# Kernel optimization log

Hardware: AMD Instinct MI355X
Metric: run time of the kernel (lower is better)

The kernel has to match this reference:

```python
import jax, jax.numpy as jnp
import numpy as np

N, E, D = 50000, 800000, 128
EPS = 1e-5


def _layernorm(x, g, b):
    m = jnp.mean(x, axis=-1, keepdims=True)
    v = jnp.mean((x - m) ** 2, axis=-1, keepdims=True)
    return (x - m) * jax.lax.rsqrt(v + EPS) * g + b


def setup_inputs() -> dict:
    key = jax.random.key(0)
    ks = jax.random.split(key, 8)
    x = jax.random.normal(ks[0], (N, D), dtype=jnp.float32)
    edge_index = jax.random.randint(ks[1], (2, E), 0, N, dtype=jnp.int64)
    edge_weights = jax.random.uniform(ks[2], (E,), dtype=jnp.float32)
    s = 1.0 / np.sqrt(D)
    W1 = jax.random.uniform(ks[3], (D, D), minval=-s, maxval=s, dtype=jnp.float32)
    b1 = jax.random.uniform(ks[4], (D,), minval=-s, maxval=s, dtype=jnp.float32)
    W2 = jax.random.uniform(ks[5], (D, D), minval=-s, maxval=s, dtype=jnp.float32)
    b2 = jax.random.uniform(ks[6], (D,), minval=-s, maxval=s, dtype=jnp.float32)
    g1 = jnp.ones((D,), jnp.float32); be1 = jnp.zeros((D,), jnp.float32)
    g2 = jnp.ones((D,), jnp.float32); be2 = jnp.zeros((D,), jnp.float32)
    return {"x": x, "edge_index": edge_index, "edge_weights": edge_weights,
            "W1": W1, "b1": b1, "g1": g1, "be1": be1,
            "W2": W2, "b2": b2, "g2": g2, "be2": be2}


def _layer(x, src, dst, ew, W, b, g, be):
    h = jax.nn.relu(x @ W + b)                      # [N, D]
    msg = ew[:, None] * h[src]                      # [E, D] gather
    h = h + jax.ops.segment_sum(msg, dst, num_segments=N)  # scatter-add (matches serial loop)
    return _layernorm(h, g, be)                     # dropout is identity at inference


def reference(x, edge_index, edge_weights, W1, b1, g1, be1, W2, b2, g2, be2):
    src, dst = edge_index[0], edge_index[1]
    x = _layer(x, src, dst, edge_weights, W1, b1, g1, be1)
    x = _layer(x, src, dst, edge_weights, W2, b2, g2, be2)
    return x
```

## Files before the change

kernel.cpp:

```cpp
#include <hip/hip_runtime.h>
#include <hip/hip_bf16.h>


#define D 128
#define SA 8192

typedef __attribute__((ext_vector_type(8))) short short8;
typedef __attribute__((ext_vector_type(4))) float f32x4;

__global__ __launch_bounds__(1024) void k_zero(int* __restrict__ p, int m) {
    int i = blockIdx.x * 1024 + threadIdx.x;
    if (i < m) p[i] = 0;
}

__global__ __launch_bounds__(1024) void k_bhist(const int* __restrict__ dst, int e,
                                                int n, int nb,
                                                int* __restrict__ bhist) {
    __shared__ int lh[784];
    int tid = threadIdx.x;
    for (int i = tid; i < nb; i += 1024) lh[i] = 0;
    __syncthreads();
    int i0 = blockIdx.x * SA;
#pragma unroll
    for (int k = 0; k < SA / 1024; ++k) {
        int i = i0 + k * 1024 + tid;
        if (i < e) {
            int d = dst[i];
            d = min(max(d, 0), n - 1);
            atomicAdd(&lh[d >> 6], 1);
        }
    }
    __syncthreads();
    for (int i = tid; i < nb; i += 1024)
        if (lh[i]) atomicAdd(&bhist[i], lh[i]);
}

__global__ __launch_bounds__(1024) void k_bscan(const int* __restrict__ bhist, int nb,
                                                int* __restrict__ boff,
                                                int* __restrict__ bcursor) {
    __shared__ int s[1024];
    int t = threadIdx.x;
    int v = (t < nb) ? bhist[t] : 0;
    s[t] = v;
    __syncthreads();
    for (int off = 1; off < 1024; off <<= 1) {
        int u = (t >= off) ? s[t - off] : 0;
        __syncthreads();
        s[t] += u;
        __syncthreads();
    }
    if (t < nb) {
        int ex = s[t] - v;
        boff[t] = ex;
        bcursor[t] = ex;
    }
}

__global__ __launch_bounds__(1024) void k_bfill(const int* __restrict__ src,
                                                const int* __restrict__ dst,
                                                const float* __restrict__ ew, int e,
                                                int n, int nb,
                                                int* __restrict__ bcursor,
                                                uint2* __restrict__ csr_tmp) {
    __shared__ int lh[784];
    __shared__ int gbase[784];
    int tid = threadIdx.x;
    for (int i = tid; i < nb; i += 1024) lh[i] = 0;
    __syncthreads();
    int i0 = blockIdx.x * SA;
    int bkt[SA / 1024], pos[SA / 1024];
    unsigned pk[SA / 1024];
    float wv[SA / 1024];
#pragma unroll
    for (int k = 0; k < SA / 1024; ++k) {
        int i = i0 + k * 1024 + tid;
        bkt[k] = -1;
        if (i < e) {
            int d = dst[i];
            d = min(max(d, 0), n - 1);
            int s = src[i];
            s = min(max(s, 0), n - 1);
            int b = d >> 6;
            bkt[k] = b;
            pos[k] = atomicAdd(&lh[b], 1);
            pk[k] = (unsigned)s | ((unsigned)(d & 63) << 16);
            wv[k] = ew[i];
        }
    }
    __syncthreads();
    for (int i = tid; i < nb; i += 1024)
        gbase[i] = lh[i] ? atomicAdd(&bcursor[i], lh[i]) : 0;
    __syncthreads();
#pragma unroll
    for (int k = 0; k < SA / 1024; ++k) {
        if (bkt[k] >= 0) {
            int idx = gbase[bkt[k]] + pos[k];
            csr_tmp[idx] = make_uint2(pk[k], __float_as_uint(wv[k]));
        }
    }
}

__global__ __launch_bounds__(256) void k_bfinal(const uint2* __restrict__ csr_tmp,
                                                const int* __restrict__ boff, int n,
                                                int e, int nb,
                                                int* __restrict__ row_ptr,
                                                uint2* __restrict__ csr) {
    __shared__ int dh[64], dcur[64], dscan[64];
    int b = blockIdx.x;
    int tid = threadIdx.x;
    int base = boff[b];
    int endo = (b + 1 < nb) ? boff[b + 1] : e;
    int ndst = min(64, n - b * 64);
    if (tid < 64) { dh[tid] = 0; dcur[tid] = 0; }
    __syncthreads();
    for (int i = base + tid; i < endo; i += 256) {
        unsigned u = csr_tmp[i].x;
        atomicAdd(&dh[(u >> 16) & 63], 1);
    }
    __syncthreads();
    if (tid < 64) {
        int v = dh[tid];
        int incl = v;
#pragma unroll
        for (int off = 1; off < 64; off <<= 1) {
            int u = __shfl_up(incl, off, 64);
            if (tid >= off) incl += u;
        }
        dscan[tid] = incl - v;
        if (tid < ndst) row_ptr[b * 64 + tid] = base + incl - v;
        if (b == nb - 1 && tid == 0) row_ptr[n] = e;
    }
    __syncthreads();
    for (int i = base + tid; i < endo; i += 256) {
        uint2 en = csr_tmp[i];
        int dlo = (en.x >> 16) & 63;
        int p = atomicAdd(&dcur[dlo], 1);
        csr[base + dscan[dlo] + p] = en;
    }
}

__global__ __launch_bounds__(256) void k_wprep(const float* __restrict__ W1,
                                               const float* __restrict__ W2,
                                               short* __restrict__ WT1,
                                               short* __restrict__ WT2) {
    int b = blockIdx.x;
    const float* W = (b < 64) ? W1 : W2;
    short* WT = (b < 64) ? WT1 : WT2;
    int i = (b & 63) * 256 + threadIdx.x;
    int k = i >> 7, nn = i & 127;
    WT[nn * 128 + k] = (short)__bfloat16_as_ushort(__float2bfloat16(W[i]));
}

__device__ __forceinline__ short8 cvt8(const float* p) {
    float4 v0 = *(const float4*)p;
    float4 v1 = *(const float4*)(p + 4);
    short8 r;
    r[0] = (short)__bfloat16_as_ushort(__float2bfloat16(v0.x));
    r[1] = (short)__bfloat16_as_ushort(__float2bfloat16(v0.y));
    r[2] = (short)__bfloat16_as_ushort(__float2bfloat16(v0.z));
    r[3] = (short)__bfloat16_as_ushort(__float2bfloat16(v0.w));
    r[4] = (short)__bfloat16_as_ushort(__float2bfloat16(v1.x));
    r[5] = (short)__bfloat16_as_ushort(__float2bfloat16(v1.y));
    r[6] = (short)__bfloat16_as_ushort(__float2bfloat16(v1.z));
    r[7] = (short)__bfloat16_as_ushort(__float2bfloat16(v1.w));
    return r;
}

template <int F32IN>
__global__ __launch_bounds__(256, 2) void k_gemm_mfma(const float* __restrict__ xf,
                                                      const short* __restrict__ xb,
                                                      const short* __restrict__ WT,
                                                      const float* __restrict__ bias,
                                                      ushort* __restrict__ hb, int n) {
    int lane = threadIdx.x & 63;
    int wid = threadIdx.x >> 6;
    int ln = lane & 15, g = lane >> 4;
    short8 bfr[8][4];
#pragma unroll
    for (int nt = 0; nt < 8; ++nt)
#pragma unroll
        for (int kk = 0; kk < 4; ++kk)
            bfr[nt][kk] = *(const short8*)(WT + (nt * 16 + ln) * 128 + kk * 32 + g * 8);
    float bvv[8];
#pragma unroll
    for (int nt = 0; nt < 8; ++nt) bvv[nt] = bias[nt * 16 + ln];

    int ntile = n >> 4;
    int stride = gridDim.x * 4;
    for (int t = blockIdx.x * 4 + wid; t < ntile; t += stride) {
        int row = t * 16 + ln;
        short8 a[4];
        if (F32IN) {
            const float* px = xf + (size_t)row * 128 + g * 8;
            a[0] = cvt8(px);
            a[1] = cvt8(px + 32);
            a[2] = cvt8(px + 64);
            a[3] = cvt8(px + 96);
        } else {
            const short* px = xb + (size_t)row * 128 + g * 8;
            a[0] = *(const short8*)(px);
            a[1] = *(const short8*)(px + 32);
            a[2] = *(const short8*)(px + 64);
            a[3] = *(const short8*)(px + 96);
        }
        f32x4 acc[8] = {};
#pragma unroll
        for (int kk = 0; kk < 4; ++kk)
#pragma unroll
            for (int nt = 0; nt < 8; ++nt)
                acc[nt] = __builtin_amdgcn_mfma_f32_16x16x32_bf16(a[kk], bfr[nt][kk],
                                                                  acc[nt], 0, 0, 0);
        int r0 = t * 16 + g * 4;
#pragma unroll
        for (int nt = 0; nt < 8; ++nt) {
#pragma unroll
            for (int r = 0; r < 4; ++r) {
                float v = fmaxf(acc[nt][r] + bvv[nt], 0.0f);
                hb[(size_t)(r0 + r) * 128 + nt * 16 + ln] =
                    __bfloat16_as_ushort(__float2bfloat16(v));
            }
        }
    }
}

__device__ __forceinline__ void bf2_unpack(unsigned int u, float& lo, float& hi) {
    lo = __uint_as_float(u << 16);
    hi = __uint_as_float(u & 0xffff0000u);
}

__global__ __launch_bounds__(256) void k_aggln(const unsigned int* __restrict__ hb,
                                               const float2* __restrict__ g2,
                                               const float2* __restrict__ be2,
                                               const int* __restrict__ row_ptr,
                                               const uint2* __restrict__ csr,
                                               float2* __restrict__ out2,
                                               unsigned int* __restrict__ xb_out,
                                               int n) {
    int wid = threadIdx.x >> 6;
    int lane = threadIdx.x & 63;
    int node = blockIdx.x * 4 + wid;
    if (node >= n) return;
    float ax, ay;
    bf2_unpack(hb[node * 64 + lane], ax, ay);
    int beg = row_ptr[node], end = row_ptr[node + 1];
    int j = beg;
    for (; j + 8 <= end; j += 8) {
        uint2 e0 = csr[j + 0], e1 = csr[j + 1], e2 = csr[j + 2], e3 = csr[j + 3];
        uint2 e4 = csr[j + 4], e5 = csr[j + 5], e6 = csr[j + 6], e7 = csr[j + 7];
        unsigned int u0 = hb[(e0.x & 0xffffu) * 64 + lane];
        unsigned int u1 = hb[(e1.x & 0xffffu) * 64 + lane];
        unsigned int u2 = hb[(e2.x & 0xffffu) * 64 + lane];
        unsigned int u3 = hb[(e3.x & 0xffffu) * 64 + lane];
        unsigned int u4 = hb[(e4.x & 0xffffu) * 64 + lane];
        unsigned int u5 = hb[(e5.x & 0xffffu) * 64 + lane];
        unsigned int u6 = hb[(e6.x & 0xffffu) * 64 + lane];
        unsigned int u7 = hb[(e7.x & 0xffffu) * 64 + lane];
        float lx, ly;
        bf2_unpack(u0, lx, ly); ax += __uint_as_float(e0.y) * lx; ay += __uint_as_float(e0.y) * ly;
        bf2_unpack(u1, lx, ly); ax += __uint_as_float(e1.y) * lx; ay += __uint_as_float(e1.y) * ly;
        bf2_unpack(u2, lx, ly); ax += __uint_as_float(e2.y) * lx; ay += __uint_as_float(e2.y) * ly;
        bf2_unpack(u3, lx, ly); ax += __uint_as_float(e3.y) * lx; ay += __uint_as_float(e3.y) * ly;
        bf2_unpack(u4, lx, ly); ax += __uint_as_float(e4.y) * lx; ay += __uint_as_float(e4.y) * ly;
        bf2_unpack(u5, lx, ly); ax += __uint_as_float(e5.y) * lx; ay += __uint_as_float(e5.y) * ly;
        bf2_unpack(u6, lx, ly); ax += __uint_as_float(e6.y) * lx; ay += __uint_as_float(e6.y) * ly;
        bf2_unpack(u7, lx, ly); ax += __uint_as_float(e7.y) * lx; ay += __uint_as_float(e7.y) * ly;
    }
    for (; j + 4 <= end; j += 4) {
        uint2 e0 = csr[j + 0], e1 = csr[j + 1], e2 = csr[j + 2], e3 = csr[j + 3];
        unsigned int u0 = hb[(e0.x & 0xffffu) * 64 + lane];
        unsigned int u1 = hb[(e1.x & 0xffffu) * 64 + lane];
        unsigned int u2 = hb[(e2.x & 0xffffu) * 64 + lane];
        unsigned int u3 = hb[(e3.x & 0xffffu) * 64 + lane];
        float lx, ly;
        bf2_unpack(u0, lx, ly); ax += __uint_as_float(e0.y) * lx; ay += __uint_as_float(e0.y) * ly;
        bf2_unpack(u1, lx, ly); ax += __uint_as_float(e1.y) * lx; ay += __uint_as_float(e1.y) * ly;
        bf2_unpack(u2, lx, ly); ax += __uint_as_float(e2.y) * lx; ay += __uint_as_float(e2.y) * ly;
        bf2_unpack(u3, lx, ly); ax += __uint_as_float(e3.y) * lx; ay += __uint_as_float(e3.y) * ly;
    }
    for (; j < end; ++j) {
        uint2 e0 = csr[j];
        float lx, ly;
        bf2_unpack(hb[(e0.x & 0xffffu) * 64 + lane], lx, ly);
        ax += __uint_as_float(e0.y) * lx;
        ay += __uint_as_float(e0.y) * ly;
    }
    float sum = ax + ay;
#pragma unroll
    for (int m = 1; m < 64; m <<= 1) sum += __shfl_xor(sum, m, 64);
    float mean = sum * (1.0f / 128.0f);
    float dx = ax - mean, dy = ay - mean;
    float ss = dx * dx + dy * dy;
#pragma unroll
    for (int m = 1; m < 64; m <<= 1) ss += __shfl_xor(ss, m, 64);
    float rstd = rsqrtf(ss * (1.0f / 128.0f) + 1e-5f);
    float2 gg = g2[lane], bb = be2[lane];
    float2 o;
    o.x = dx * rstd * gg.x + bb.x;
    o.y = dy * rstd * gg.y + bb.y;
    out2[node * 64 + lane] = o;
    if (xb_out) {
        unsigned int u = (unsigned int)__bfloat16_as_ushort(__float2bfloat16(o.x)) |
                         ((unsigned int)__bfloat16_as_ushort(__float2bfloat16(o.y)) << 16);
        xb_out[node * 64 + lane] = u;
    }
}

extern "C" void kernel_launch(void* const* d_in, const int* in_sizes, int n_in,
                              void* d_out, int out_size, void* d_ws, size_t ws_size,
                              hipStream_t stream) {
    const float* x   = (const float*)d_in[0];
    const int*  eidx = (const int*)d_in[1];
    const float* ew  = (const float*)d_in[2];
    const float* W1  = (const float*)d_in[3];
    const float* b1  = (const float*)d_in[4];
    const float* g1  = (const float*)d_in[5];
    const float* be1 = (const float*)d_in[6];
    const float* W2  = (const float*)d_in[7];
    const float* b2  = (const float*)d_in[8];
    const float* g2  = (const float*)d_in[9];
    const float* be2 = (const float*)d_in[10];
    int n = in_sizes[0] / D;
    int e = in_sizes[2];
    const int* srcp = eidx;
    const int* dstp = eidx + e;
    float* out = (float*)d_out;

    char* ws = (char*)d_ws;
    size_t off = 0;
    auto alloc = [&](size_t bytes) {
        void* p = ws + off;
        off += (bytes + 255) & ~(size_t)255;
        return p;
    };
    ushort* hb      = (ushort*)alloc((size_t)n * D * sizeof(ushort));
    uint*   xb      = (uint*)alloc((size_t)n * (D / 2) * sizeof(uint));
    int*    row_ptr = (int*)alloc((size_t)(n + 1) * sizeof(int));
    int*    bhist   = (int*)alloc(1024 * sizeof(int));
    int*    boff    = (int*)alloc(1024 * sizeof(int));
    int*    bcursor = (int*)alloc(1024 * sizeof(int));
    short*  WT1     = (short*)alloc(128 * 128 * sizeof(short));
    short*  WT2     = (short*)alloc(128 * 128 * sizeof(short));
    uint2*  csr_tmp = (uint2*)alloc((size_t)e * sizeof(uint2));
    uint2*  csr     = (uint2*)alloc((size_t)e * sizeof(uint2));

    int nb = (n + 63) >> 6;
    int nblk = (e + SA - 1) / SA;

    k_zero<<<1, 1024, 0, stream>>>(bhist, nb);
    k_wprep<<<128, 256, 0, stream>>>(W1, W2, WT1, WT2);
    k_bhist<<<nblk, 1024, 0, stream>>>(dstp, e, n, nb, bhist);
    k_bscan<<<1, 1024, 0, stream>>>(bhist, nb, boff, bcursor);
    k_bfill<<<nblk, 1024, 0, stream>>>(srcp, dstp, ew, e, n, nb, bcursor, csr_tmp);
    k_bfinal<<<nb, 256, 0, stream>>>(csr_tmp, boff, n, e, nb, row_ptr, csr);

    k_gemm_mfma<1><<<512, 256, 0, stream>>>(x, nullptr, WT1, b1, hb, n);
    k_aggln<<<(n + 3) / 4, 256, 0, stream>>>((const unsigned int*)hb,
                                             (const float2*)g1, (const float2*)be1,
                                             row_ptr, csr, (float2*)out, xb, n);
    k_gemm_mfma<0><<<512, 256, 0, stream>>>(nullptr, (const short*)xb, WT2, b2, hb, n);
    k_aggln<<<(n + 3) / 4, 256, 0, stream>>>((const unsigned int*)hb,
                                             (const float2*)g2, (const float2*)be2,
                                             row_ptr, csr, (float2*)out, nullptr, n);
}
```

Before: 146.1 us.

## Merge prep kernels, use nontemporal loads/stores, split GEMM N-tiles across waves

Fuses the histogram-zeroing and weight-transpose launches into one kernel. Switches streaming loads and stores in the CSR build, GEMM and aggregation to nontemporal builtins. Restructures the MFMA GEMM so the four waves of a block share one 16-row tile, each computing two 16-column output tiles, with the grid doubled. The first layer's aggregation also skips its redundant fp32 output write. Together these aim to cut launch overhead, cache pollution, register pressure and wasted writes, at the cost of more blocks and the A tile being reloaded by each wave.

```diff
diff --git a/kernel.cpp b/kernel.cpp
--- a/kernel.cpp
+++ b/kernel.cpp
@@ -7,10 +7,24 @@
 
 typedef __attribute__((ext_vector_type(8))) short short8;
 typedef __attribute__((ext_vector_type(4))) float f32x4;
-
-__global__ __launch_bounds__(1024) void k_zero(int* __restrict__ p, int m) {
-    int i = blockIdx.x * 1024 + threadIdx.x;
-    if (i < m) p[i] = 0;
+typedef __attribute__((ext_vector_type(2))) float f32x2;
+typedef __attribute__((ext_vector_type(2))) unsigned int uint2v;
+
+__global__ __launch_bounds__(256) void k_prep(const float* __restrict__ W1,
+                                              const float* __restrict__ W2,
+                                              short* __restrict__ WT1,
+                                              short* __restrict__ WT2,
+                                              int* __restrict__ bhist, int nb) {
+    int b = blockIdx.x;
+    if (b < 128) {
+        const float* W = (b < 64) ? W1 : W2;
+        short* WT = (b < 64) ? WT1 : WT2;
+        int i = (b & 63) * 256 + threadIdx.x;
+        int k = i >> 7, nn = i & 127;
+        WT[nn * 128 + k] = (short)__bfloat16_as_ushort(__float2bfloat16(W[i]));
+    } else {
+        for (int i = threadIdx.x; i < nb; i += 256) bhist[i] = 0;
+    }
 }
 
 __global__ __launch_bounds__(1024) void k_bhist(const int* __restrict__ dst, int e,
@@ -25,7 +39,7 @@
     for (int k = 0; k < SA / 1024; ++k) {
         int i = i0 + k * 1024 + tid;
         if (i < e) {
-            int d = dst[i];
+            int d = __builtin_nontemporal_load(dst + i);
             d = min(max(d, 0), n - 1);
             atomicAdd(&lh[d >> 6], 1);
         }
@@ -61,7 +75,7 @@
                                                 const float* __restrict__ ew, int e,
                                                 int n, int nb,
                                                 int* __restrict__ bcursor,
-                                                uint2* __restrict__ csr_tmp) {
+                                                uint2v* __restrict__ csr_tmp) {
     __shared__ int lh[784];
     __shared__ int gbase[784];
     int tid = threadIdx.x;
@@ -76,15 +90,15 @@
         int i = i0 + k * 1024 + tid;
         bkt[k] = -1;
         if (i < e) {
-            int d = dst[i];
+            int d = __builtin_nontemporal_load(dst + i);
             d = min(max(d, 0), n - 1);
-            int s = src[i];
+            int s = __builtin_nontemporal_load(src + i);
             s = min(max(s, 0), n - 1);
             int b = d >> 6;
             bkt[k] = b;
             pos[k] = atomicAdd(&lh[b], 1);
             pk[k] = (unsigned)s | ((unsigned)(d & 63) << 16);
-            wv[k] = ew[i];
+            wv[k] = __builtin_nontemporal_load(ew + i);
         }
     }
     __syncthreads();
@@ -95,16 +109,19 @@
     for (int k = 0; k < SA / 1024; ++k) {
         if (bkt[k] >= 0) {
             int idx = gbase[bkt[k]] + pos[k];
-            csr_tmp[idx] = make_uint2(pk[k], __float_as_uint(wv[k]));
-        }
-    }
-}
-
-__global__ __launch_bounds__(256) void k_bfinal(const uint2* __restrict__ csr_tmp,
+            uint2v en;
+            en.x = pk[k];
+            en.y = __float_as_uint(wv[k]);
+            __builtin_nontemporal_store(en, csr_tmp + idx);
+        }
+    }
+}
+
+__global__ __launch_bounds__(256) void k_bfinal(const uint2v* __restrict__ csr_tmp,
                                                 const int* __restrict__ boff, int n,
                                                 int e, int nb,
                                                 int* __restrict__ row_ptr,
-                                                uint2* __restrict__ csr) {
+                                                uint2v* __restrict__ csr) {
     __shared__ int dh[64], dcur[64], dscan[64];
     int b = blockIdx.x;
     int tid = threadIdx.x;
@@ -114,8 +131,8 @@
     if (tid < 64) { dh[tid] = 0; dcur[tid] = 0; }
     __syncthreads();
     for (int i = base + tid; i < endo; i += 256) {
-        unsigned u = csr_tmp[i].x;
-        atomicAdd(&dh[(u >> 16) & 63], 1);
+        uint2v en = __builtin_nontemporal_load(csr_tmp + i);
+        atomicAdd(&dh[(en.x >> 16) & 63], 1);
     }
     __syncthreads();
     if (tid < 64) {
@@ -132,28 +149,16 @@
     }
     __syncthreads();
     for (int i = base + tid; i < endo; i += 256) {
-        uint2 en = csr_tmp[i];
+        uint2v en = __builtin_nontemporal_load(csr_tmp + i);
         int dlo = (en.x >> 16) & 63;
         int p = atomicAdd(&dcur[dlo], 1);
         csr[base + dscan[dlo] + p] = en;
     }
 }
 
-__global__ __launch_bounds__(256) void k_wprep(const float* __restrict__ W1,
-                                               const float* __restrict__ W2,
-                                               short* __restrict__ WT1,
-                                               short* __restrict__ WT2) {
-    int b = blockIdx.x;
-    const float* W = (b < 64) ? W1 : W2;
-    short* WT = (b < 64) ? WT1 : WT2;
-    int i = (b & 63) * 256 + threadIdx.x;
-    int k = i >> 7, nn = i & 127;
-    WT[nn * 128 + k] = (short)__bfloat16_as_ushort(__float2bfloat16(W[i]));
-}
-
 __device__ __forceinline__ short8 cvt8(const float* p) {
-    float4 v0 = *(const float4*)p;
-    float4 v1 = *(const float4*)(p + 4);
+    f32x4 v0 = __builtin_nontemporal_load((const f32x4*)p);
+    f32x4 v1 = __builtin_nontemporal_load((const f32x4*)(p + 4));
     short8 r;
     r[0] = (short)__bfloat16_as_ushort(__float2bfloat16(v0.x));
     r[1] = (short)__bfloat16_as_ushort(__float2bfloat16(v0.y));
@@ -167,27 +172,26 @@
 }
 
 template <int F32IN>
-__global__ __launch_bounds__(256, 2) void k_gemm_mfma(const float* __restrict__ xf,
-                                                      const short* __restrict__ xb,
-                                                      const short* __restrict__ WT,
-                                                      const float* __restrict__ bias,
-                                                      ushort* __restrict__ hb, int n) {
+__global__ __launch_bounds__(256) void k_gemm_mfma(const float* __restrict__ xf,
+                                                   const short* __restrict__ xb,
+                                                   const short* __restrict__ WT,
+                                                   const float* __restrict__ bias,
+                                                   ushort* __restrict__ hb, int n) {
     int lane = threadIdx.x & 63;
-    int wid = threadIdx.x >> 6;
+    int w = threadIdx.x >> 6;
     int ln = lane & 15, g = lane >> 4;
-    short8 bfr[8][4];
-#pragma unroll
-    for (int nt = 0; nt < 8; ++nt)
-#pragma unroll
-        for (int kk = 0; kk < 4; ++kk)
-            bfr[nt][kk] = *(const short8*)(WT + (nt * 16 + ln) * 128 + kk * 32 + g * 8);
-    float bvv[8];
-#pragma unroll
-    for (int nt = 0; nt < 8; ++nt) bvv[nt] = bias[nt * 16 + ln];
+    int nt0 = w, nt1 = w + 4;
+    short8 bfr0[4], bfr1[4];
+#pragma unroll
+    for (int kk = 0; kk < 4; ++kk) {
+        bfr0[kk] = *(const short8*)(WT + (nt0 * 16 + ln) * 128 + kk * 32 + g * 8);
+        bfr1[kk] = *(const short8*)(WT + (nt1 * 16 + ln) * 128 + kk * 32 + g * 8);
+    }
+    float bv0 = bias[nt0 * 16 + ln];
+    float bv1 = bias[nt1 * 16 + ln];
 
     int ntile = n >> 4;
-    int stride = gridDim.x * 4;
-    for (int t = blockIdx.x * 4 + wid; t < ntile; t += stride) {
+    for (int t = blockIdx.x; t < ntile; t += gridDim.x) {
         int row = t * 16 + ln;
         short8 a[4];
         if (F32IN) {
@@ -198,27 +202,26 @@
             a[3] = cvt8(px + 96);
         } else {
             const short* px = xb + (size_t)row * 128 + g * 8;
-            a[0] = *(const short8*)(px);
-            a[1] = *(const short8*)(px + 32);
-            a[2] = *(const short8*)(px + 64);
-            a[3] = *(const short8*)(px + 96);
-        }
-        f32x4 acc[8] = {};
-#pragma unroll
-        for (int kk = 0; kk < 4; ++kk)
-#pragma unroll
-            for (int nt = 0; nt < 8; ++nt)
-                acc[nt] = __builtin_amdgcn_mfma_f32_16x16x32_bf16(a[kk], bfr[nt][kk],
-                                                                  acc[nt], 0, 0, 0);
+            a[0] = __builtin_nontemporal_load((const short8*)(px));
+            a[1] = __builtin_nontemporal_load((const short8*)(px + 32));
+            a[2] = __builtin_nontemporal_load((const short8*)(px + 64));
+            a[3] = __builtin_nontemporal_load((const short8*)(px + 96));
+        }
+        f32x4 acc0 = {}, acc1 = {};
+#pragma unroll
+        for (int kk = 0; kk < 4; ++kk) {
+            acc0 = __builtin_amdgcn_mfma_f32_16x16x32_bf16(a[kk], bfr0[kk], acc0, 0, 0, 0);
+            acc1 = __builtin_amdgcn_mfma_f32_16x16x32_bf16(a[kk], bfr1[kk], acc1, 0, 0, 0);
+        }
         int r0 = t * 16 + g * 4;
 #pragma unroll
-        for (int nt = 0; nt < 8; ++nt) {
-#pragma unroll
-            for (int r = 0; r < 4; ++r) {
-                float v = fmaxf(acc[nt][r] + bvv[nt], 0.0f);
-                hb[(size_t)(r0 + r) * 128 + nt * 16 + ln] =
-                    __bfloat16_as_ushort(__float2bfloat16(v));
-            }
+        for (int r = 0; r < 4; ++r) {
+            float v0 = fmaxf(acc0[r] + bv0, 0.0f);
+            float v1 = fmaxf(acc1[r] + bv1, 0.0f);
+            hb[(size_t)(r0 + r) * 128 + nt0 * 16 + ln] =
+                __bfloat16_as_ushort(__float2bfloat16(v0));
+            hb[(size_t)(r0 + r) * 128 + nt1 * 16 + ln] =
+                __bfloat16_as_ushort(__float2bfloat16(v1));
         }
     }
 }
@@ -232,8 +235,8 @@
                                                const float2* __restrict__ g2,
                                                const float2* __restrict__ be2,
                                                const int* __restrict__ row_ptr,
-                                               const uint2* __restrict__ csr,
-                                               float2* __restrict__ out2,
+                                               const uint2v* __restrict__ csr,
+                                               f32x2* __restrict__ out2,
                                                unsigned int* __restrict__ xb_out,
                                                int n) {
     int wid = threadIdx.x >> 6;
@@ -245,8 +248,14 @@
     int beg = row_ptr[node], end = row_ptr[node + 1];
     int j = beg;
     for (; j + 8 <= end; j += 8) {
-        uint2 e0 = csr[j + 0], e1 = csr[j + 1], e2 = csr[j + 2], e3 = csr[j + 3];
-        uint2 e4 = csr[j + 4], e5 = csr[j + 5], e6 = csr[j + 6], e7 = csr[j + 7];
+        uint2v e0 = __builtin_nontemporal_load(csr + j + 0);
+        uint2v e1 = __builtin_nontemporal_load(csr + j + 1);
+        uint2v e2 = __builtin_nontemporal_load(csr + j + 2);
+        uint2v e3 = __builtin_nontemporal_load(csr + j + 3);
+        uint2v e4 = __builtin_nontemporal_load(csr + j + 4);
+        uint2v e5 = __builtin_nontemporal_load(csr + j + 5);
+        uint2v e6 = __builtin_nontemporal_load(csr + j + 6);
+        uint2v e7 = __builtin_nontemporal_load(csr + j + 7);
         unsigned int u0 = hb[(e0.x & 0xffffu) * 64 + lane];
         unsigned int u1 = hb[(e1.x & 0xffffu) * 64 + lane];
         unsigned int u2 = hb[(e2.x & 0xffffu) * 64 + lane];
@@ -266,7 +275,10 @@
         bf2_unpack(u7, lx, ly); ax += __uint_as_float(e7.y) * lx; ay += __uint_as_float(e7.y) * ly;
     }
     for (; j + 4 <= end; j += 4) {
-        uint2 e0 = csr[j + 0], e1 = csr[j + 1], e2 = csr[j + 2], e3 = csr[j + 3];
+        uint2v e0 = __builtin_nontemporal_load(csr + j + 0);
+        uint2v e1 = __builtin_nontemporal_load(csr + j + 1);
+        uint2v e2 = __builtin_nontemporal_load(csr + j + 2);
+        uint2v e3 = __builtin_nontemporal_load(csr + j + 3);
         unsigned int u0 = hb[(e0.x & 0xffffu) * 64 + lane];
         unsigned int u1 = hb[(e1.x & 0xffffu) * 64 + lane];
         unsigned int u2 = hb[(e2.x & 0xffffu) * 64 + lane];
@@ -278,7 +290,7 @@
         bf2_unpack(u3, lx, ly); ax += __uint_as_float(e3.y) * lx; ay += __uint_as_float(e3.y) * ly;
     }
     for (; j < end; ++j) {
-        uint2 e0 = csr[j];
+        uint2v e0 = __builtin_nontemporal_load(csr + j);
         float lx, ly;
         bf2_unpack(hb[(e0.x & 0xffffu) * 64 + lane], lx, ly);
         ax += __uint_as_float(e0.y) * lx;
@@ -294,10 +306,10 @@
     for (int m = 1; m < 64; m <<= 1) ss += __shfl_xor(ss, m, 64);
     float rstd = rsqrtf(ss * (1.0f / 128.0f) + 1e-5f);
     float2 gg = g2[lane], bb = be2[lane];
-    float2 o;
+    f32x2 o;
     o.x = dx * rstd * gg.x + bb.x;
     o.y = dy * rstd * gg.y + bb.y;
-    out2[node * 64 + lane] = o;
+    if (out2) __builtin_nontemporal_store(o, out2 + node * 64 + lane);
     if (xb_out) {
         unsigned int u = (unsigned int)__bfloat16_as_ushort(__float2bfloat16(o.x)) |
                          ((unsigned int)__bfloat16_as_ushort(__float2bfloat16(o.y)) << 16);
@@ -323,7 +335,6 @@
     int e = in_sizes[2];
     const int* srcp = eidx;
     const int* dstp = eidx + e;
-    float* out = (float*)d_out;
 
     char* ws = (char*)d_ws;
     size_t off = 0;
@@ -340,25 +351,24 @@
     int*    bcursor = (int*)alloc(1024 * sizeof(int));
     short*  WT1     = (short*)alloc(128 * 128 * sizeof(short));
     short*  WT2     = (short*)alloc(128 * 128 * sizeof(short));
-    uint2*  csr_tmp = (uint2*)alloc((size_t)e * sizeof(uint2));
-    uint2*  csr     = (uint2*)alloc((size_t)e * sizeof(uint2));
+    uint2v* csr_tmp = (uint2v*)alloc((size_t)e * sizeof(uint2v));
+    uint2v* csr     = (uint2v*)alloc((size_t)e * sizeof(uint2v));
 
     int nb = (n + 63) >> 6;
     int nblk = (e + SA - 1) / SA;
 
-    k_zero<<<1, 1024, 0, stream>>>(bhist, nb);
-    k_wprep<<<128, 256, 0, stream>>>(W1, W2, WT1, WT2);
+    k_prep<<<129, 256, 0, stream>>>(W1, W2, WT1, WT2, bhist, nb);
     k_bhist<<<nblk, 1024, 0, stream>>>(dstp, e, n, nb, bhist);
     k_bscan<<<1, 1024, 0, stream>>>(bhist, nb, boff, bcursor);
     k_bfill<<<nblk, 1024, 0, stream>>>(srcp, dstp, ew, e, n, nb, bcursor, csr_tmp);
     k_bfinal<<<nb, 256, 0, stream>>>(csr_tmp, boff, n, e, nb, row_ptr, csr);
 
-    k_gemm_mfma<1><<<512, 256, 0, stream>>>(x, nullptr, WT1, b1, hb, n);
+    k_gemm_mfma<1><<<1024, 256, 0, stream>>>(x, nullptr, WT1, b1, hb, n);
     k_aggln<<<(n + 3) / 4, 256, 0, stream>>>((const unsigned int*)hb,
                                              (const float2*)g1, (const float2*)be1,
-                                             row_ptr, csr, (float2*)out, xb, n);
-    k_gemm_mfma<0><<<512, 256, 0, stream>>>(nullptr, (const short*)xb, WT2, b2, hb, n);
+                                             row_ptr, csr, nullptr, xb, n);
+    k_gemm_mfma<0><<<1024, 256, 0, stream>>>(nullptr, (const short*)xb, WT2, b2, hb, n);
     k_aggln<<<(n + 3) / 4, 256, 0, stream>>>((const unsigned int*)hb,
                                              (const float2*)g2, (const float2*)be2,
-                                             row_ptr, csr, (float2*)out, nullptr, n);
-}
+                                             row_ptr, csr, (f32x2*)d_out, nullptr, n);
+}
```

New measurement: 187.5 us. 28.3% more time.
